# Performance work log

Measured on AMD Instinct MI355X. Metric: run time of the kernel, lower is better.

Reference implementation:

```python
import jax, jax.numpy as jnp
import numpy as np

N = 50000      # nodes
M = 800000     # edges
D = 128        # node_state_dim == msg_dim
EF = 32        # edge_feat_dim
DF = 32        # node_dist_feat_dim
ATT = 128      # att_hidden_dim
L = 2          # num_layer (num_prop = 1)
IN = D + EF + DF  # 192, MLP input dim


def setup_inputs() -> dict:
    key = jax.random.key(0)
    ks = jax.random.split(key, 18)
    rn = lambda k, shape, s=0.05: jax.random.normal(k, shape, dtype=jnp.float32) * s
    return {
        "node_feat":   rn(ks[0], (N, D), 1.0),
        "node_feat_c": rn(ks[1], (N, D), 1.0),
        "edge":        jax.random.randint(ks[2], (M, 2), 0, N, dtype=jnp.int32),
        "edge_feat":   rn(ks[3], (M, EF), 1.0),
        "dist_feat":   rn(ks[4], (M, DF), 1.0),
        # msg MLP: Linear(IN->D) -> ReLU -> Linear(D->D), stacked over layers
        "msg_w0": rn(ks[5], (L, IN, D)),  "msg_b0": jnp.zeros((L, D), jnp.float32),
        "msg_w1": rn(ks[6], (L, D, D)),   "msg_b1": jnp.zeros((L, D), jnp.float32),
        # attention head: Linear(IN->ATT) -> ReLU -> Linear(ATT->D) -> Sigmoid
        "att_w0": rn(ks[7], (L, IN, ATT)), "att_b0": jnp.zeros((L, ATT), jnp.float32),
        "att_w1": rn(ks[8], (L, ATT, D)),  "att_b1": jnp.zeros((L, D), jnp.float32),
        # LSTMCell params (torch layout: W_ih [4H, in], W_hh [4H, H], gate order i,f,g,o)
        "lstm_wih": rn(ks[9],  (L, 4 * D, D)),
        "lstm_whh": rn(ks[10], (L, 4 * D, D)),
        "lstm_bih": jnp.zeros((L, 4 * D), jnp.float32),
        "lstm_bhh": jnp.zeros((L, 4 * D), jnp.float32),
    }


def _lstm_cell(x, h, c, wih, whh, bih, bhh):
    gates = x @ wih.T + bih + h @ whh.T + bhh          # [N, 4D]
    i, f, g, o = jnp.split(gates, 4, axis=1)
    c2 = jax.nn.sigmoid(f) * c + jax.nn.sigmoid(i) * jnp.tanh(g)
    h2 = jax.nn.sigmoid(o) * jnp.tanh(c2)
    return h2, c2


def reference(node_feat, node_feat_c, edge, edge_feat, dist_feat,
              msg_w0, msg_b0, msg_w1, msg_b1,
              att_w0, att_b0, att_w1, att_b1,
              lstm_wih, lstm_whh, lstm_bih, lstm_bhh):
    src = edge[:, 0]
    dst = edge[:, 1]
    state, state_c = node_feat, node_feat_c
    for ii in range(L):
        if ii > 0:
            state = jax.nn.relu(state)
        # _prop (num_prop = 1)
        state_diff = state[src] - state[dst]                               # [M, D]
        edge_input = jnp.concatenate([state_diff, edge_feat, dist_feat], 1)  # [M, IN]
        msg = jax.nn.relu(edge_input @ msg_w0[ii] + msg_b0[ii]) @ msg_w1[ii] + msg_b1[ii]
        att = jax.nn.sigmoid(
            jax.nn.relu(edge_input @ att_w0[ii] + att_b0[ii]) @ att_w1[ii] + att_b1[ii])
        msg = msg * att
        state_msg = jax.ops.segment_sum(msg, dst, num_segments=N)          # scatter_add
        state, state_c = _lstm_cell(state_msg, state, state_c,
                                    lstm_wih[ii], lstm_whh[ii],
                                    lstm_bih[ii], lstm_bhh[ii])
    return state
```

## Files before the change

kernel.cpp:

```cpp
#include <hip/hip_runtime.h>
#include <hip/hip_bf16.h>

constexpr int N  = 50000;
constexpr int M  = 800000;
constexpr int D  = 128;
constexpr int IN = 192;
constexpr int TE = 64;
constexpr int NCH = 20;
constexpr int NBLK = (N + 255) / 256;

typedef __attribute__((ext_vector_type(4)))  short short4v;
typedef __attribute__((ext_vector_type(8)))  short short8;
typedef __attribute__((ext_vector_type(16))) float f32x16;

__device__ __align__(16) short g_wp[163840];
__device__ __align__(16) short g_lw[262144];
__device__ __align__(16) short g_efdf[(size_t)M * 64];
__device__ __align__(16) short g_sbf[(size_t)N * D];
__device__ int g_cnt[N];
__device__ int g_part[NBLK];
__device__ int g_ssrc[M];
__device__ int g_sdst[M];
__device__ int g_inv[M];

__device__ __forceinline__ float sigm(float x) { return 1.0f / (1.0f + __expf(-x)); }

__device__ __forceinline__ short f2bf(float f) {
    unsigned u = __builtin_bit_cast(unsigned, f);
    u = (u + 0x7FFFu + ((u >> 16) & 1u)) >> 16;
    return (short)u;
}
__device__ __forceinline__ float bf2f(short s) {
    return __builtin_bit_cast(float, ((unsigned)(unsigned short)s) << 16);
}
__device__ __forceinline__ unsigned pk2(float a, float b) {
    __hip_bfloat162 h = __float22bfloat162_rn(float2{a, b});
    unsigned u;
    __builtin_memcpy(&u, &h, 4);
    return u;
}

__global__ void zero_cnt_kernel() {
    for (int i = blockIdx.x * 256 + threadIdx.x; i < N; i += gridDim.x * 256) g_cnt[i] = 0;
}
__global__ void hist_kernel(const int* __restrict__ edge) {
    int e = blockIdx.x * 256 + threadIdx.x;
    if (e < M) atomicAdd(&g_cnt[edge[e * 2 + 1]], 1);
}
__global__ void scanA_kernel() {
    __shared__ int red[256];
    const int t = threadIdx.x;
    const int idx = blockIdx.x * 256 + t;
    red[t] = (idx < N) ? g_cnt[idx] : 0;
    __syncthreads();
#pragma unroll
    for (int s = 128; s > 0; s >>= 1) {
        if (t < s) red[t] += red[t + s];
        __syncthreads();
    }
    if (t == 0) g_part[blockIdx.x] = red[0];
}
__global__ void scanB_kernel() {
    __shared__ int sh[256];
    const int t = threadIdx.x;
    int v = (t < NBLK) ? g_part[t] : 0;
    sh[t] = v;
    __syncthreads();
    int x = v;
    for (int s = 1; s < 256; s <<= 1) {
        int y = (t >= s) ? sh[t - s] : 0;
        __syncthreads();
        x += y; sh[t] = x;
        __syncthreads();
    }
    if (t < NBLK) g_part[t] = x - v;
}
__global__ void scanC_kernel() {
    __shared__ int sh[256];
    const int t = threadIdx.x;
    const int idx = blockIdx.x * 256 + t;
    int v = (idx < N) ? g_cnt[idx] : 0;
    sh[t] = v;
    __syncthreads();
    int x = v;
    for (int s = 1; s < 256; s <<= 1) {
        int y = (t >= s) ? sh[t - s] : 0;
        __syncthreads();
        x += y; sh[t] = x;
        __syncthreads();
    }
    if (idx < N) g_cnt[idx] = g_part[blockIdx.x] + x - v;
}
__global__ void scatter_kernel(const int* __restrict__ edge) {
    int e = blockIdx.x * 256 + threadIdx.x;
    if (e < M) {
        const int s = edge[e * 2], d = edge[e * 2 + 1];
        const int p = atomicAdd(&g_cnt[d], 1);
        g_ssrc[p] = s;
        g_sdst[p] = d;
        g_inv[p]  = e;
    }
}

__global__ void pack_edge(const float* __restrict__ w0m, const float* __restrict__ w0a,
                          const float* __restrict__ w1m, const float* __restrict__ w1a) {
    int gid = blockIdx.x * 256 + threadIdx.x;
    int ii = gid / 81920;
    int r  = gid % 81920;
    int p  = r / 40960;  r %= 40960;
    int which = (r >= 24576) ? 1 : 0;
    int r2 = which ? r - 24576 : r;
    int e    = r2 & 7;
    int f    = r2 >> 3;
    int lane = f & 63;
    int ktct = f >> 6;
    int ct = ktct & 3, kt = ktct >> 2;
    int k   = kt * 16 + ((lane >> 5) << 3) + e;
    int col = ct * 32 + (lane & 31);
    const float* w0 = p ? w0a : w0m;
    const float* w1 = p ? w1a : w1m;
    float v = which ? w1[((size_t)ii * D + k) * D + col]
                    : w0[((size_t)ii * IN + k) * D + col];
    g_wp[gid] = f2bf(v);
}

__global__ void pack_lstm(const float* __restrict__ wih, const float* __restrict__ whh) {
    int gid = blockIdx.x * 256 + threadIdx.x;
    int ii = gid >> 17;
    int r  = gid & 131071;
    int e = r & 7, f = r >> 3;
    int lane = f & 63, rest = f >> 6;
    int cf = rest & 15, kt = rest >> 4;
    int col = cf * 32 + (lane & 31);
    int k   = (kt & 7) * 16 + ((lane >> 5) << 3) + e;
    const float* src = (kt < 8) ? wih : whh;
    g_lw[gid] = f2bf(src[((size_t)ii * 512 + col) * D + k]);
}

__global__ void pack_efdf(const float* __restrict__ ef, const float* __restrict__ df) {
    int gid = blockIdx.x * 256 + threadIdx.x;
    int p = gid >> 3, c0 = (gid & 7) * 8;
    const int e = g_inv[p];
    const float* s = (c0 < 32) ? (ef + (size_t)e * 32 + c0) : (df + (size_t)e * 32 + (c0 - 32));
    float4 u0 = *(const float4*)s, u1 = *(const float4*)(s + 4);
    short8 t;
    unsigned* tp = (unsigned*)&t;
    tp[0] = pk2(u0.x, u0.y); tp[1] = pk2(u0.z, u0.w);
    tp[2] = pk2(u1.x, u1.y); tp[3] = pk2(u1.z, u1.w);
    *(short8*)(g_efdf + (size_t)gid * 8) = t;
}

__global__ void init_kernel(const float4* __restrict__ nf, const float4* __restrict__ nfc,
                            float4* __restrict__ state, float4* __restrict__ state_c) {
    const int total = N * D / 4;
    for (int i = blockIdx.x * blockDim.x + threadIdx.x; i < total; i += gridDim.x * blockDim.x) {
        state[i]   = nf[i];
        state_c[i] = nfc[i];
    }
}

__global__ void prep_kernel(float4* __restrict__ state, float4* __restrict__ msg, int do_relu) {
    const int total = N * D / 4;
    const float4 z = make_float4(0.f, 0.f, 0.f, 0.f);
    for (int i = blockIdx.x * blockDim.x + threadIdx.x; i < total; i += gridDim.x * blockDim.x) {
        float4 v = state[i];
        if (do_relu) {
            v.x = fmaxf(v.x, 0.f); v.y = fmaxf(v.y, 0.f);
            v.z = fmaxf(v.z, 0.f); v.w = fmaxf(v.w, 0.f);
            state[i] = v;
        }
        short4v b;
        unsigned* bp = (unsigned*)&b;
        bp[0] = pk2(v.x, v.y); bp[1] = pk2(v.z, v.w);
        *(short4v*)(g_sbf + (size_t)i * 4) = b;
        msg[i] = z;
    }
}

__device__ __forceinline__ void stage_ld(const short8* __restrict__ gsrc, int gc, short8 g[2], int tid) {
    const short8* p = gsrc + (size_t)gc * 512;
    g[0] = p[tid]; g[1] = p[tid + 256];
}
__device__ __forceinline__ void stage_st(short8* wb, int gc, const short8 g[2], int tid) {
    short8* d = wb + (gc & 1) * 512;
    d[tid] = g[0]; d[tid + 256] = g[1];
}

#define MFMA(a, b, c) __builtin_amdgcn_mfma_f32_32x32x16_bf16(a, b, c, 0, 0, 0)

template<int BASE>
__device__ __forceinline__ void gemmA(const short8* __restrict__ gsrc, short8* wb,
                                      const short8 a1[12], int tid, int lane, int cg,
                                      f32x16& o0, f32x16& o1) {
    f32x16 acc0 = {}, acc1 = {};
#pragma unroll
    for (int c = 0; c < 6; ++c) {
        const int gc = BASE + c;
        short8 g[2];
        if (gc + 1 < NCH) stage_ld(gsrc, gc + 1, g, tid);
        const short8* buf = wb + (gc & 1) * 512;
#pragma unroll
        for (int kl = 0; kl < 2; ++kl) {
            short8 b0 = buf[(kl * 4 + cg * 2 + 0) * 64 + lane];
            short8 b1 = buf[(kl * 4 + cg * 2 + 1) * 64 + lane];
            acc0 = MFMA(a1[c * 2 + kl], b0, acc0);
            acc1 = MFMA(a1[c * 2 + kl], b1, acc1);
        }
        if (gc + 1 < NCH) stage_st(wb, gc + 1, g, tid);
        __syncthreads();
    }
    o0 = acc0; o1 = acc1;
}

template<int BASE>
__device__ __forceinline__ void gemmH(const short8* __restrict__ gsrc, short8* wb,
                                      const short (*hsr)[136], int tid, int lane, int cg, int half,
                                      f32x16& o0, f32x16& o1) {
    f32x16 acc0 = {}, acc1 = {};
#pragma unroll
    for (int c = 0; c < 4; ++c) {
        const int gc = BASE + c;
        short8 g[2];
        if (gc + 1 < NCH) stage_ld(gsrc, gc + 1, g, tid);
        const short8* buf = wb + (gc & 1) * 512;
#pragma unroll
        for (int kl = 0; kl < 2; ++kl) {
            const int kt = c * 2 + kl;
            short8 a2 = *(const short8*)&hsr[lane & 31][kt * 16 + half];
            short8 b0 = buf[(kl * 4 + cg * 2 + 0) * 64 + lane];
            short8 b1 = buf[(kl * 4 + cg * 2 + 1) * 64 + lane];
            acc0 = MFMA(a2, b0, acc0);
            acc1 = MFMA(a2, b1, acc1);
        }
        if (gc + 1 < NCH) stage_st(wb, gc + 1, g, tid);
        __syncthreads();
    }
    o0 = acc0; o1 = acc1;
}

__device__ __forceinline__ void hwrite(short (*hsr)[136], const f32x16& a0, const f32x16& a1v,
                                       const float* __restrict__ b0, int lane, int cg) {
#pragma unroll
    for (int ct = 0; ct < 2; ++ct) {
        const int col = cg * 64 + ct * 32 + (lane & 31);
        const float bv = b0[col];
        f32x16 a = ct ? a1v : a0;
#pragma unroll
        for (int rp = 0; rp < 8; ++rp) {
            const int reg = rp * 2;
            const int row = (reg & 3) + 8 * (reg >> 2) + 4 * (lane >> 5);
            const unsigned pr = pk2(fmaxf(a[reg] + bv, 0.f), fmaxf(a[reg + 1] + bv, 0.f));
            hsr[row][col]     = (short)(pr & 0xFFFF);
            hsr[row + 1][col] = (short)(pr >> 16);
        }
    }
}

__global__ __launch_bounds__(256, 4)
void edge_mfma(int ii,
               const float* __restrict__ b0m, const float* __restrict__ b1m,
               const float* __restrict__ b0a, const float* __restrict__ b1a,
               float* __restrict__ state_msg) {
    __shared__ __align__(16) char pool[34048];
    short8* wb = (short8*)pool;
    short (*hs)[32][136] = (short(*)[32][136])(pool + 16384);
    int* sdst = (int*)(pool + 33792);

    const int tid  = threadIdx.x;
    const int lane = tid & 63;
    const int w    = tid >> 6;
    const int rt   = w >> 1, cg = w & 1;
    const int e0   = blockIdx.x * TE;

    if (tid < TE) sdst[tid] = g_sdst[e0 + tid];

    const int er   = e0 + rt * 32 + (lane & 31);
    const int half = (lane >> 5) << 3;
    const int s  = g_ssrc[er];
    const int d2 = g_sdst[er];
    const short* srow = g_sbf + (size_t)s  * D;
    const short* drow = g_sbf + (size_t)d2 * D;
    short8 a1[12];
#pragma unroll
    for (int kt = 0; kt < 8; ++kt) {
        const int k0 = kt * 16 + half;
        short8 sv = *(const short8*)(srow + k0);
        short8 dv = *(const short8*)(drow + k0);
        short8 t;
        unsigned* tp = (unsigned*)&t;
#pragma unroll
        for (int i = 0; i < 4; ++i)
            tp[i] = pk2(bf2f(sv[2 * i])     - bf2f(dv[2 * i]),
                        bf2f(sv[2 * i + 1]) - bf2f(dv[2 * i + 1]));
        a1[kt] = t;
    }
#pragma unroll
    for (int kt = 8; kt < 12; ++kt)
        a1[kt] = *(const short8*)(g_efdf + (size_t)er * 64 + (kt - 8) * 16 + half);

    const short8* gsrc = (const short8*)(g_wp + (size_t)ii * 81920);

    {
        short8 g[2];
        stage_ld(gsrc, 0, g, tid);
        stage_st(wb, 0, g, tid);
        __syncthreads();
    }

    f32x16 t0, t1, m0, m1, c0, c1;
    gemmA<0>(gsrc, wb, a1, tid, lane, cg, t0, t1);
    hwrite(hs[rt], t0, t1, b0m, lane, cg);
    __syncthreads();
    gemmH<6>(gsrc, wb, hs[rt], tid, lane, cg, half, m0, m1);
    gemmA<10>(gsrc, wb, a1, tid, lane, cg, t0, t1);
    hwrite(hs[rt], t0, t1, b0a, lane, cg);
    __syncthreads();
    gemmH<16>(gsrc, wb, hs[rt], tid, lane, cg, half, c0, c1);

    float (*vt)[D] = (float(*)[D])pool;
#pragma unroll
    for (int ct = 0; ct < 2; ++ct) {
        const int col = cg * 64 + ct * 32 + (lane & 31);
        const float bm = b1m[col], ba = b1a[col];
        f32x16 mv = ct ? m1 : m0;
        f32x16 av = ct ? c1 : c0;
#pragma unroll
        for (int reg = 0; reg < 16; ++reg) {
            const int row = rt * 32 + (reg & 3) + 8 * (reg >> 2) + 4 * (lane >> 5);
            vt[row][col] = (mv[reg] + bm) * sigm(av[reg] + ba);
        }
    }
    __syncthreads();

    const int colr = tid & 127;
    const int rbase = (tid >> 7) * 32;
    float run = 0.f;
    int cur = sdst[rbase];
#pragma unroll 4
    for (int r = 0; r < 32; ++r) {
        const int dd = sdst[rbase + r];
        if (dd != cur) {
            atomicAdd(state_msg + (size_t)cur * D + colr, run);
            run = 0.f; cur = dd;
        }
        run += vt[rbase + r][colr];
    }
    atomicAdd(state_msg + (size_t)cur * D + colr, run);
}

__global__ __launch_bounds__(256, 4)
void lstm_mfma(const float* __restrict__ x, float* __restrict__ hbuf, float* __restrict__ cbuf,
               int ii,
               const float* __restrict__ bih, const float* __restrict__ bhh) {
    __shared__ short8 wb[2048];
    const int tid  = threadIdx.x;
    const int lane = tid & 63;
    const int w    = tid >> 6;
    const int n0   = blockIdx.x * 32;
    const int half = (lane >> 5) << 3;
    const int nl   = lane & 31;
    const int nld  = min(n0 + nl, N - 1);

    const short8* gsrc = (const short8*)(g_lw + (size_t)ii * 131072);

    {
        short8 g[4];
#pragma unroll
        for (int i = 0; i < 4; ++i) g[i] = gsrc[tid + i * 256];
#pragma unroll
        for (int i = 0; i < 4; ++i) wb[tid + i * 256] = g[i];
        __syncthreads();
    }

    f32x16 acc[4] = {};
#pragma unroll
    for (int kt = 0; kt < 16; ++kt) {
        const float* srow = (kt < 8) ? (x + (size_t)nld * D + kt * 16 + half)
                                     : (hbuf + (size_t)nld * D + (kt - 8) * 16 + half);
        float4 u0 = *(const float4*)(srow);
        float4 u1 = *(const float4*)(srow + 4);
        short8 a;
        unsigned* ap = (unsigned*)&a;
        ap[0] = pk2(u0.x, u0.y); ap[1] = pk2(u0.z, u0.w);
        ap[2] = pk2(u1.x, u1.y); ap[3] = pk2(u1.z, u1.w);

        short8 g[4];
        if (kt + 1 < 16) {
            const short8* p = gsrc + (size_t)(kt + 1) * 1024;
#pragma unroll
            for (int i = 0; i < 4; ++i) g[i] = p[tid + i * 256];
        }
        const short8* buf = wb + (kt & 1) * 1024;
#pragma unroll
        for (int q = 0; q < 4; ++q) {
            short8 b = buf[(q * 4 + w) * 64 + lane];
            acc[q] = MFMA(a, b, acc[q]);
        }
        if (kt + 1 < 16) {
            short8* d = wb + ((kt + 1) & 1) * 1024;
#pragma unroll
            for (int i = 0; i < 4; ++i) d[tid + i * 256] = g[i];
        }
        __syncthreads();
    }

    const int col = (w << 5) + nl;
    const float bi = bih[col]       + bhh[col];
    const float bf = bih[128 + col] + bhh[128 + col];
    const float bg = bih[256 + col] + bhh[256 + col];
    const float bo = bih[384 + col] + bhh[384 + col];
#pragma unroll
    for (int reg = 0; reg < 16; ++reg) {
        const int nn = (reg & 3) + 8 * (reg >> 2) + 4 * (lane >> 5);
        const int n = n0 + nn;
        if (n < N) {
            const float gi = acc[0][reg] + bi;
            const float gf = acc[1][reg] + bf;
            const float gg = acc[2][reg] + bg;
            const float go = acc[3][reg] + bo;
            float* cp = cbuf + (size_t)n * D + col;
            const float c2 = sigm(gf) * (*cp) + sigm(gi) * tanhf(gg);
            const float h2 = sigm(go) * tanhf(c2);
            *cp = c2;
            hbuf[(size_t)n * D + col] = h2;
        }
    }
}

extern "C" void kernel_launch(void* const* d_in, const int* in_sizes, int n_in,
                              void* d_out, int out_size, void* d_ws, size_t ws_size,
                              hipStream_t stream) {
    const float* node_feat   = (const float*)d_in[0];
    const float* node_feat_c = (const float*)d_in[1];
    const int*   edge        = (const int*)d_in[2];
    const float* edge_feat   = (const float*)d_in[3];
    const float* dist_feat   = (const float*)d_in[4];
    const float* msg_w0 = (const float*)d_in[5];
    const float* msg_b0 = (const float*)d_in[6];
    const float* msg_w1 = (const float*)d_in[7];
    const float* msg_b1 = (const float*)d_in[8];
    const float* att_w0 = (const float*)d_in[9];
    const float* att_b0 = (const float*)d_in[10];
    const float* att_w1 = (const float*)d_in[11];
    const float* att_b1 = (const float*)d_in[12];
    const float* lstm_wih = (const float*)d_in[13];
    const float* lstm_whh = (const float*)d_in[14];
    const float* lstm_bih = (const float*)d_in[15];
    const float* lstm_bhh = (const float*)d_in[16];

    float* state     = (float*)d_out;
    float* state_c   = (float*)d_ws;
    float* state_msg = (float*)d_ws + (size_t)N * D;

    zero_cnt_kernel<<<256, 256, 0, stream>>>();
    hist_kernel<<<(M + 255) / 256, 256, 0, stream>>>(edge);
    scanA_kernel<<<NBLK, 256, 0, stream>>>();
    scanB_kernel<<<1, 256, 0, stream>>>();
    scanC_kernel<<<NBLK, 256, 0, stream>>>();
    scatter_kernel<<<(M + 255) / 256, 256, 0, stream>>>(edge);

    pack_efdf<<<25000, 256, 0, stream>>>(edge_feat, dist_feat);
    pack_edge<<<640, 256, 0, stream>>>(msg_w0, att_w0, msg_w1, att_w1);
    pack_lstm<<<1024, 256, 0, stream>>>(lstm_wih, lstm_whh);

    init_kernel<<<2048, 256, 0, stream>>>((const float4*)node_feat, (const float4*)node_feat_c,
                                          (float4*)state, (float4*)state_c);

    for (int ii = 0; ii < 2; ++ii) {
        prep_kernel<<<2048, 256, 0, stream>>>((float4*)state, (float4*)state_msg, ii > 0 ? 1 : 0);

        edge_mfma<<<M / TE, 256, 0, stream>>>(
            ii,
            msg_b0 + (size_t)ii * D, msg_b1 + (size_t)ii * D,
            att_b0 + (size_t)ii * D, att_b1 + (size_t)ii * D,
            state_msg);

        lstm_mfma<<<(N + 31) / 32, 256, 0, stream>>>(
            state_msg, state, state_c, ii,
            lstm_bih + (size_t)ii * 4 * D, lstm_bhh + (size_t)ii * 4 * D);
    }
}
```

Measured before the change: 931.4 us.

## Double edge tile to 128 per 512-thread block sharing staged weight chunks

Doubles the edge tile to 128 edges per block with 512 threads, so each staged weight chunk in LDS is reused by eight waves instead of four. Each thread now loads one weight vector per chunk instead of two. The msg result is kept in registers as packed bf16 so LDS can be reused, and the final scale-and-scatter runs in two passes of 64 rows. This halves per-edge weight-staging traffic but uses more LDS and registers per block, lowers occupancy, and rounds msg to bf16 before the multiply.

```diff
diff --git a/kernel.cpp b/kernel.cpp
--- a/kernel.cpp
+++ b/kernel.cpp
@@ -5,7 +5,7 @@
 constexpr int M  = 800000;
 constexpr int D  = 128;
 constexpr int IN = 192;
-constexpr int TE = 64;
+constexpr int TE = 128;
 constexpr int NCH = 20;
 constexpr int NBLK = (N + 255) / 256;
 
@@ -177,15 +177,6 @@
     }
 }
 
-__device__ __forceinline__ void stage_ld(const short8* __restrict__ gsrc, int gc, short8 g[2], int tid) {
-    const short8* p = gsrc + (size_t)gc * 512;
-    g[0] = p[tid]; g[1] = p[tid + 256];
-}
-__device__ __forceinline__ void stage_st(short8* wb, int gc, const short8 g[2], int tid) {
-    short8* d = wb + (gc & 1) * 512;
-    d[tid] = g[0]; d[tid + 256] = g[1];
-}
-
 #define MFMA(a, b, c) __builtin_amdgcn_mfma_f32_32x32x16_bf16(a, b, c, 0, 0, 0)
 
 template<int BASE>
@@ -196,8 +187,8 @@
 #pragma unroll
     for (int c = 0; c < 6; ++c) {
         const int gc = BASE + c;
-        short8 g[2];
-        if (gc + 1 < NCH) stage_ld(gsrc, gc + 1, g, tid);
+        short8 g;
+        if (gc + 1 < NCH) g = gsrc[(size_t)(gc + 1) * 512 + tid];
         const short8* buf = wb + (gc & 1) * 512;
 #pragma unroll
         for (int kl = 0; kl < 2; ++kl) {
@@ -206,7 +197,7 @@
             acc0 = MFMA(a1[c * 2 + kl], b0, acc0);
             acc1 = MFMA(a1[c * 2 + kl], b1, acc1);
         }
-        if (gc + 1 < NCH) stage_st(wb, gc + 1, g, tid);
+        if (gc + 1 < NCH) wb[((gc + 1) & 1) * 512 + tid] = g;
         __syncthreads();
     }
     o0 = acc0; o1 = acc1;
@@ -220,8 +211,8 @@
 #pragma unroll
     for (int c = 0; c < 4; ++c) {
         const int gc = BASE + c;
-        short8 g[2];
-        if (gc + 1 < NCH) stage_ld(gsrc, gc + 1, g, tid);
+        short8 g;
+        if (gc + 1 < NCH) g = gsrc[(size_t)(gc + 1) * 512 + tid];
         const short8* buf = wb + (gc & 1) * 512;
 #pragma unroll
         for (int kl = 0; kl < 2; ++kl) {
@@ -232,7 +223,7 @@
             acc0 = MFMA(a2, b0, acc0);
             acc1 = MFMA(a2, b1, acc1);
         }
-        if (gc + 1 < NCH) stage_st(wb, gc + 1, g, tid);
+        if (gc + 1 < NCH) wb[((gc + 1) & 1) * 512 + tid] = g;
         __syncthreads();
     }
     o0 = acc0; o1 = acc1;
@@ -256,20 +247,21 @@
     }
 }
 
-__global__ __launch_bounds__(256, 4)
+__global__ __launch_bounds__(512, 4)
 void edge_mfma(int ii,
                const float* __restrict__ b0m, const float* __restrict__ b1m,
                const float* __restrict__ b0a, const float* __restrict__ b1a,
                float* __restrict__ state_msg) {
-    __shared__ __align__(16) char pool[34048];
+    __shared__ __align__(16) char pool[51712];
     short8* wb = (short8*)pool;
     short (*hs)[32][136] = (short(*)[32][136])(pool + 16384);
-    int* sdst = (int*)(pool + 33792);
+    int* sdst = (int*)(pool + 51200);
 
     const int tid  = threadIdx.x;
     const int lane = tid & 63;
     const int w    = tid >> 6;
-    const int rt   = w >> 1, cg = w & 1;
+    const int rt   = w >> 1;
+    const int cg   = w & 1;
     const int e0   = blockIdx.x * TE;
 
     if (tid < TE) sdst[tid] = g_sdst[e0 + tid];
@@ -300,52 +292,67 @@
 
     const short8* gsrc = (const short8*)(g_wp + (size_t)ii * 81920);
 
-    {
-        short8 g[2];
-        stage_ld(gsrc, 0, g, tid);
-        stage_st(wb, 0, g, tid);
-        __syncthreads();
-    }
+    wb[tid] = gsrc[tid];
+    __syncthreads();
 
     f32x16 t0, t1, m0, m1, c0, c1;
     gemmA<0>(gsrc, wb, a1, tid, lane, cg, t0, t1);
     hwrite(hs[rt], t0, t1, b0m, lane, cg);
     __syncthreads();
     gemmH<6>(gsrc, wb, hs[rt], tid, lane, cg, half, m0, m1);
+
+    unsigned mb[16];
+#pragma unroll
+    for (int ct = 0; ct < 2; ++ct) {
+        const float bm = b1m[cg * 64 + ct * 32 + (lane & 31)];
+        f32x16 mv = ct ? m1 : m0;
+#pragma unroll
+        for (int rp = 0; rp < 8; ++rp)
+            mb[ct * 8 + rp] = pk2(mv[rp * 2] + bm, mv[rp * 2 + 1] + bm);
+    }
+
     gemmA<10>(gsrc, wb, a1, tid, lane, cg, t0, t1);
     hwrite(hs[rt], t0, t1, b0a, lane, cg);
     __syncthreads();
     gemmH<16>(gsrc, wb, hs[rt], tid, lane, cg, half, c0, c1);
 
-    float (*vt)[D] = (float(*)[D])pool;
-#pragma unroll
-    for (int ct = 0; ct < 2; ++ct) {
-        const int col = cg * 64 + ct * 32 + (lane & 31);
-        const float bm = b1m[col], ba = b1a[col];
-        f32x16 mv = ct ? m1 : m0;
-        f32x16 av = ct ? c1 : c0;
-#pragma unroll
-        for (int reg = 0; reg < 16; ++reg) {
-            const int row = rt * 32 + (reg & 3) + 8 * (reg >> 2) + 4 * (lane >> 5);
-            vt[row][col] = (mv[reg] + bm) * sigm(av[reg] + ba);
-        }
-    }
-    __syncthreads();
-
+    float (*vt)[132] = (float(*)[132])pool;
     const int colr = tid & 127;
-    const int rbase = (tid >> 7) * 32;
-    float run = 0.f;
-    int cur = sdst[rbase];
+    const int sub  = tid >> 7;
+#pragma unroll
+    for (int pass = 0; pass < 2; ++pass) {
+        if ((rt >> 1) == pass) {
+#pragma unroll
+            for (int ct = 0; ct < 2; ++ct) {
+                const int col = cg * 64 + ct * 32 + (lane & 31);
+                const float ba = b1a[col];
+                f32x16 av = ct ? c1 : c0;
+#pragma unroll
+                for (int rp = 0; rp < 8; ++rp) {
+                    const int reg = rp * 2;
+                    const unsigned u = mb[ct * 8 + rp];
+                    const int row = (rt & 1) * 32 + (reg & 3) + 8 * (reg >> 2) + 4 * (lane >> 5);
+                    vt[row][col]     = bf2f((short)(u & 0xFFFF)) * sigm(av[reg] + ba);
+                    vt[row + 1][col] = bf2f((short)(u >> 16))    * sigm(av[reg + 1] + ba);
+                }
+            }
+        }
+        __syncthreads();
+        const int gbase = pass * 64 + sub * 16;
+        float run = 0.f;
+        int cur = sdst[gbase];
 #pragma unroll 4
-    for (int r = 0; r < 32; ++r) {
-        const int dd = sdst[rbase + r];
-        if (dd != cur) {
-            atomicAdd(state_msg + (size_t)cur * D + colr, run);
-            run = 0.f; cur = dd;
-        }
-        run += vt[rbase + r][colr];
-    }
-    atomicAdd(state_msg + (size_t)cur * D + colr, run);
+        for (int r = 0; r < 16; ++r) {
+            const int dd = sdst[gbase + r];
+            if (dd != cur) {
+                atomicAdd(state_msg + (size_t)cur * D + colr, run);
+                run = 0.f; cur = dd;
+            }
+            run += vt[sub * 16 + r][colr];
+        }
+        atomicAdd(state_msg + (size_t)cur * D + colr, run);
+        __syncthreads();
+    }
 }
 
 __global__ __launch_bounds__(256, 4)
@@ -469,7 +476,7 @@
     for (int ii = 0; ii < 2; ++ii) {
         prep_kernel<<<2048, 256, 0, stream>>>((float4*)state, (float4*)state_msg, ii > 0 ? 1 : 0);
 
-        edge_mfma<<<M / TE, 256, 0, stream>>>(
+        edge_mfma<<<M / TE, 512, 0, stream>>>(
             ii,
             msg_b0 + (size_t)ii * D, msg_b1 + (size_t)ii * D,
             att_b0 + (size_t)ii * D, att_b1 + (size_t)ii * D,
```

New measurement: 914.7 us. Within noise of the previous version (-1.8%).
